# Kernel optimization log

Measured on AMD Instinct MI355X. Metric: run time of the kernel, lower is better.

Reference implementation:

```python
import jax, jax.numpy as jnp
import numpy as np

N_EMBED = 1024
HEAD_SIZE = 128

def setup_inputs() -> dict:
    key = jax.random.key(0)
    k1, k2, k3, k4 = jax.random.split(key, 4)
    x = jax.random.normal(k1, (8, 2048, N_EMBED), dtype=jnp.float32)
    # torch.nn.Linear default init: U(-1/sqrt(in), 1/sqrt(in)); stored as [out, in],
    # we store transposed [in, out] for x @ W.
    bound = 1.0 / np.sqrt(N_EMBED)
    Wk = jax.random.uniform(k2, (N_EMBED, HEAD_SIZE), jnp.float32, -bound, bound)
    Wq = jax.random.uniform(k3, (N_EMBED, HEAD_SIZE), jnp.float32, -bound, bound)
    Wv = jax.random.uniform(k4, (N_EMBED, HEAD_SIZE), jnp.float32, -bound, bound)
    return {"x": x, "Wk": Wk, "Wq": Wq, "Wv": Wv}

def reference(x, Wk, Wq, Wv):
    # x: [B, T, E]
    k = jnp.einsum('bte,eh->bth', x, Wk)  # [B, T, H]
    q = jnp.einsum('bte,eh->bth', x, Wq)
    v = jnp.einsum('bte,eh->bth', x, Wv)
    scale = 1.0 / np.sqrt(HEAD_SIZE).astype(np.float32)
    wei = jnp.einsum('bqh,bkh->bqk', q, k) * scale  # [B, T, T]
    wei = jax.nn.softmax(wei, axis=-1)
    out = jnp.einsum('bqk,bkh->bqh', wei, v)  # [B, T, H]
    return out
```

## Files before the change

kernel.cpp:

```cpp
#include <hip/hip_runtime.h>

#define BATCH 8
#define TLEN 2048
#define EMB 1024
#define HDIM 128
#define SCALE 0.08838834764831845f
#define NSPLIT 4

typedef _Float16 f16x8 __attribute__((ext_vector_type(8)));
typedef _Float16 f16x4 __attribute__((ext_vector_type(4)));
typedef float f32x4 __attribute__((ext_vector_type(4)));

static __device__ __forceinline__ f32x4 mfma16(f16x8 a, f16x8 b, f32x4 c) {
    return __builtin_amdgcn_mfma_f32_16x16x32_f16(a, b, c, 0, 0, 0);
}

__global__ void prep_w(const float* __restrict__ Wk, const float* __restrict__ Wq,
                       const float* __restrict__ Wv, _Float16* __restrict__ wtf) {
    int g = blockIdx.x * 256 + threadIdx.x;
    int lane = g & 63;
    int kstep = (g >> 6) & 31;
    int ntile = g >> 11;
    int n = ntile * 16 + (lane & 15);
    int sel = n >> 7;
    int h = n & 127;
    const float* W = (sel == 0) ? Wk : (sel == 1) ? Wq : Wv;
    int kbase = kstep * 32 + (lane >> 4) * 8;
    f16x8 o;
#pragma unroll
    for (int j = 0; j < 8; j++) {
        float v = W[(size_t)(kbase + j) * HDIM + h];
        if (sel == 1) v *= SCALE;
        o[j] = (_Float16)v;
    }
    *(f16x8*)&wtf[(size_t)g * 8] = o;
}

#define XPITCH 1048
__global__ __launch_bounds__(256) void prep_x(const float* __restrict__ x,
                                              _Float16* __restrict__ xf) {
    __shared__ _Float16 ls[16 * XPITCH];
    const int t = threadIdx.x;
    const int mtile = blockIdx.x;
    const float* src = x + (size_t)mtile * 16 * EMB;
#pragma unroll
    for (int i = 0; i < 16; i++) {
        int f = t + i * 256;
        int row = f >> 8;
        int col = (f & 255) * 4;
        float4 v = *(const float4*)&src[(size_t)row * EMB + col];
        f16x4 h;
        h[0] = (_Float16)v.x; h[1] = (_Float16)v.y;
        h[2] = (_Float16)v.z; h[3] = (_Float16)v.w;
        *(f16x4*)&ls[row * XPITCH + col] = h;
    }
    __syncthreads();
    _Float16* dst = xf + (size_t)mtile * 32 * 512;
#pragma unroll
    for (int i = 0; i < 8; i++) {
        int u = t + i * 256;
        int kstep = u >> 6;
        int lane = u & 63;
        int kcol = kstep * 32 + (lane >> 4) * 8;
        f16x8 v = *(const f16x8*)&ls[(lane & 15) * XPITCH + kcol];
        *(f16x8*)&dst[(size_t)u * 8] = v;
    }
}

__global__ __launch_bounds__(512, 2) void proj_kernel(
        const _Float16* __restrict__ xf, const _Float16* __restrict__ wtf,
        _Float16* __restrict__ kb, _Float16* __restrict__ qb, _Float16* __restrict__ vbT) {
    const int t = threadIdx.x;
    const int wv = t >> 6;
    const int lane = t & 63;
    const int m16 = lane & 15;
    const int quad = lane >> 4;
    const int mhalf = (wv >> 2) * 32;
    const int nq = wv & 3;
    const int n0 = nq * 96;
    const int m0 = blockIdx.x * 64;

    const f32x4 zero4 = {0.f, 0.f, 0.f, 0.f};
    f32x4 acc[2][6];
#pragma unroll
    for (int mt = 0; mt < 2; mt++)
#pragma unroll
        for (int nt = 0; nt < 6; nt++) acc[mt][nt] = zero4;

    const _Float16* xq = &xf[(size_t)(blockIdx.x * 4 + (wv >> 2) * 2) * 32 * 512
                             + (size_t)lane * 8];
    const _Float16* wq = &wtf[(size_t)(nq * 6) * 32 * 512 + (size_t)lane * 8];

#pragma unroll 8
    for (int kstep = 0; kstep < 32; kstep++) {
        f16x8 af[2];
#pragma unroll
        for (int mt = 0; mt < 2; mt++)
            af[mt] = *(const f16x8*)&xq[(size_t)(mt * 32 + kstep) * 512];
        f16x8 bf[6];
#pragma unroll
        for (int nt = 0; nt < 6; nt++)
            bf[nt] = *(const f16x8*)&wq[(size_t)(nt * 32 + kstep) * 512];
#pragma unroll
        for (int nt = 0; nt < 6; nt++) {
            acc[0][nt] = mfma16(af[0], bf[nt], acc[0][nt]);
            acc[1][nt] = mfma16(af[1], bf[nt], acc[1][nt]);
        }
    }
#pragma unroll
    for (int nt = 0; nt < 6; nt++) {
        int n = n0 + nt * 16 + m16;
        int nsel = n >> 7;
        int h = n & 127;
        if (nsel < 2) {
            _Float16* dst = (nsel == 0) ? kb : qb;
#pragma unroll
            for (int mt = 0; mt < 2; mt++)
#pragma unroll
                for (int r = 0; r < 4; r++) {
                    int mg = m0 + mhalf + mt * 16 + quad * 4 + r;
                    dst[(size_t)mg * HDIM + h] = (_Float16)acc[mt][nt][r];
                }
        } else {
#pragma unroll
            for (int mt = 0; mt < 2; mt++) {
                int mg = m0 + mhalf + mt * 16 + quad * 4;
                int bb = mg >> 11, tok = mg & 2047;
                f16x4 pk;
#pragma unroll
                for (int r = 0; r < 4; r++) pk[r] = (_Float16)acc[mt][nt][r];
                *(f16x4*)&vbT[((size_t)bb * HDIM + h) * TLEN + tok] = pk;
            }
        }
    }
}

__global__ __launch_bounds__(256, 3) void attn_kernel(
        const _Float16* __restrict__ qb, const _Float16* __restrict__ kb,
        const _Float16* __restrict__ vbT,
        _Float16* __restrict__ po, float* __restrict__ pl) {
    __shared__ _Float16 kls[64 * 132];
    __shared__ _Float16 vtl[128 * 68];
    __shared__ _Float16 pls[4 * 32 * 72];
    const int t = threadIdx.x;
    const int qt = blockIdx.x;
    const int b = blockIdx.y;
    const int sp = blockIdx.z;
    const int wv = t >> 6;
    const int lane = t & 63;
    const int m16 = lane & 15;
    const int quad = lane >> 4;
    const int q0 = qt * 128 + wv * 32;
    _Float16* pw = pls + wv * (32 * 72);

    f16x8 qf[2][4];
#pragma unroll
    for (int mt = 0; mt < 2; mt++)
#pragma unroll
        for (int ks = 0; ks < 4; ks++)
            qf[mt][ks] = *(const f16x8*)
                &qb[((size_t)b * TLEN + q0 + mt * 16 + m16) * HDIM + ks * 32 + quad * 8];

    const f32x4 zero4 = {0.f, 0.f, 0.f, 0.f};
    f32x4 o[2][8];
    float lacc[2] = {0.f, 0.f};
#pragma unroll
    for (int mt = 0; mt < 2; mt++)
#pragma unroll
        for (int nt = 0; nt < 8; nt++) o[mt][nt] = zero4;

    for (int kt = sp * 8; kt < sp * 8 + 8; kt++) {
        const int k0 = kt * 64;
        f16x8 kreg[4];
#pragma unroll
        for (int rep = 0; rep < 4; rep++) {
            int u = t + rep * 256;
            kreg[rep] = *(const f16x8*)
                &kb[((size_t)b * TLEN + k0 + (u >> 4)) * HDIM + (u & 15) * 8];
        }
        __syncthreads();
#pragma unroll
        for (int rep = 0; rep < 4; rep++) {
            int u = t + rep * 256;
            *(f16x8*)&kls[(u >> 4) * 132 + (u & 15) * 8] = kreg[rep];
        }
#pragma unroll
        for (int rep = 0; rep < 4; rep++) {
            int u = t + rep * 256;
            f16x8 v = *(const f16x8*)
                &vbT[((size_t)b * HDIM + (u >> 3)) * TLEN + k0 + (u & 7) * 8];
            *(f16x8*)&vtl[(u >> 3) * 68 + (u & 7) * 8] = v;
        }
        __syncthreads();
#pragma unroll
        for (int kt_ = 0; kt_ < 4; kt_++) {
            f32x4 st0 = zero4, st1 = zero4;
#pragma unroll
            for (int ks = 0; ks < 4; ks++) {
                f16x8 kf = *(const f16x8*)&kls[(kt_ * 16 + m16) * 132 + ks * 32 + quad * 8];
                st0 = mfma16(kf, qf[0][ks], st0);
                st1 = mfma16(kf, qf[1][ks], st1);
            }
            f16x4 p0, p1;
#pragma unroll
            for (int r = 0; r < 4; r++) {
                float e0 = __expf(st0[r]);
                float e1 = __expf(st1[r]);
                lacc[0] += e0;
                lacc[1] += e1;
                p0[r] = (_Float16)e0;
                p1[r] = (_Float16)e1;
            }
            *(f16x4*)&pw[m16 * 72 + kt_ * 16 + quad * 4] = p0;
            *(f16x4*)&pw[(16 + m16) * 72 + kt_ * 16 + quad * 4] = p1;
        }
        f16x8 ap[2][2];
#pragma unroll
        for (int mt = 0; mt < 2; mt++)
#pragma unroll
            for (int kc = 0; kc < 2; kc++)
                ap[mt][kc] = *(const f16x8*)&pw[(mt * 16 + m16) * 72 + kc * 32 + quad * 8];
#pragma unroll
        for (int nt = 0; nt < 8; nt++) {
            f16x8 b0 = *(const f16x8*)&vtl[(nt * 16 + m16) * 68 + quad * 8];
            f16x8 b1 = *(const f16x8*)&vtl[(nt * 16 + m16) * 68 + 32 + quad * 8];
            o[0][nt] = mfma16(ap[0][0], b0, o[0][nt]);
            o[0][nt] = mfma16(ap[0][1], b1, o[0][nt]);
            o[1][nt] = mfma16(ap[1][0], b0, o[1][nt]);
            o[1][nt] = mfma16(ap[1][1], b1, o[1][nt]);
        }
    }
#pragma unroll
    for (int mt = 0; mt < 2; mt++) {
        lacc[mt] += __shfl_xor(lacc[mt], 16);
        lacc[mt] += __shfl_xor(lacc[mt], 32);
    }
#pragma unroll
    for (int mt = 0; mt < 2; mt++) {
        if (quad == 0)
            pl[((size_t)(sp * BATCH + b)) * TLEN + q0 + mt * 16 + m16] = lacc[mt];
#pragma unroll
        for (int r = 0; r < 4; r++) {
            int row = q0 + mt * 16 + quad * 4 + r;
            size_t prow = ((size_t)(sp * BATCH + b)) * TLEN + row;
#pragma unroll
            for (int nt = 0; nt < 8; nt++)
                po[prow * HDIM + nt * 16 + m16] = (_Float16)o[mt][nt][r];
        }
    }
}

__global__ void combine_kernel(const _Float16* __restrict__ po, const float* __restrict__ pl,
                               float* __restrict__ out) {
    int g = blockIdx.x * 256 + threadIdx.x;
    int row = g >> 5;
    int part = g & 31;
    int bb = row >> 11;
    int tok = row & 2047;
    float L = 0.f;
    float4 acc = {0.f, 0.f, 0.f, 0.f};
#pragma unroll
    for (int s = 0; s < NSPLIT; s++) {
        size_t prow = ((size_t)(s * BATCH + bb)) * TLEN + tok;
        L += pl[prow];
        f16x4 p = *(const f16x4*)&po[prow * HDIM + part * 4];
        acc.x += (float)p[0]; acc.y += (float)p[1];
        acc.z += (float)p[2]; acc.w += (float)p[3];
    }
    float inv = 1.f / L;
    float4 res = {acc.x * inv, acc.y * inv, acc.z * inv, acc.w * inv};
    *(float4*)&out[(size_t)row * HDIM + part * 4] = res;
}

extern "C" void kernel_launch(void* const* d_in, const int* in_sizes, int n_in,
                              void* d_out, int out_size, void* d_ws, size_t ws_size,
                              hipStream_t stream) {
    const float* x  = (const float*)d_in[0];
    const float* Wk = (const float*)d_in[1];
    const float* Wq = (const float*)d_in[2];
    const float* Wv = (const float*)d_in[3];
    float* out = (float*)d_out;
    char* ws = (char*)d_ws;
    _Float16* wtf = (_Float16*)(ws);
    _Float16* xf  = (_Float16*)(ws + (1ull << 20));
    _Float16* kb  = (_Float16*)(ws + (33ull << 20));
    _Float16* qb  = (_Float16*)(ws + (37ull << 20));
    _Float16* vbT = (_Float16*)(ws + (41ull << 20));
    _Float16* po  = (_Float16*)(ws + (45ull << 20));
    float* pl = (float*)(ws + (61ull << 20));

    prep_w<<<dim3(192), dim3(256), 0, stream>>>(Wk, Wq, Wv, wtf);
    prep_x<<<dim3(1024), dim3(256), 0, stream>>>(x, xf);
    proj_kernel<<<dim3(256), dim3(512), 0, stream>>>(xf, wtf, kb, qb, vbT);
    attn_kernel<<<dim3(16, BATCH, NSPLIT), dim3(256), 0, stream>>>(qb, kb, vbT, po, pl);
    combine_kernel<<<dim3(2048), dim3(256), 0, stream>>>(po, pl, out);
}
```

Measured before the change: 163.9 us.

## Merge prep kernels, read K directly from global, repack split-K partial layout

Merges the weight and input conversion kernels into one launch to save a launch gap. The attention kernel drops the K tile from shared memory and reads K fragments straight from global memory, freeing LDS so occupancy can rise to 4 blocks per CU. Partial outputs are stored in an MFMA-fragment-native layout with contiguous 16-byte stores, and the combine kernel is rewritten to read that layout. The trade-off is that every wave now reloads K from global/L2 instead of sharing it, and the final output writes in combine become scattered scalar stores.

New measurement: 222.0 us. 35.4% more time.

```diff
diff --git a/kernel.cpp b/kernel.cpp
--- a/kernel.cpp
+++ b/kernel.cpp
@@ -15,55 +15,56 @@
     return __builtin_amdgcn_mfma_f32_16x16x32_f16(a, b, c, 0, 0, 0);
 }
 
-__global__ void prep_w(const float* __restrict__ Wk, const float* __restrict__ Wq,
-                       const float* __restrict__ Wv, _Float16* __restrict__ wtf) {
-    int g = blockIdx.x * 256 + threadIdx.x;
-    int lane = g & 63;
-    int kstep = (g >> 6) & 31;
-    int ntile = g >> 11;
-    int n = ntile * 16 + (lane & 15);
-    int sel = n >> 7;
-    int h = n & 127;
-    const float* W = (sel == 0) ? Wk : (sel == 1) ? Wq : Wv;
-    int kbase = kstep * 32 + (lane >> 4) * 8;
-    f16x8 o;
-#pragma unroll
-    for (int j = 0; j < 8; j++) {
-        float v = W[(size_t)(kbase + j) * HDIM + h];
-        if (sel == 1) v *= SCALE;
-        o[j] = (_Float16)v;
-    }
-    *(f16x8*)&wtf[(size_t)g * 8] = o;
-}
-
 #define XPITCH 1048
-__global__ __launch_bounds__(256) void prep_x(const float* __restrict__ x,
-                                              _Float16* __restrict__ xf) {
+__global__ __launch_bounds__(256) void prep_kernel(
+        const float* __restrict__ x, const float* __restrict__ Wk,
+        const float* __restrict__ Wq, const float* __restrict__ Wv,
+        _Float16* __restrict__ xf, _Float16* __restrict__ wtf) {
     __shared__ _Float16 ls[16 * XPITCH];
     const int t = threadIdx.x;
-    const int mtile = blockIdx.x;
-    const float* src = x + (size_t)mtile * 16 * EMB;
-#pragma unroll
-    for (int i = 0; i < 16; i++) {
-        int f = t + i * 256;
-        int row = f >> 8;
-        int col = (f & 255) * 4;
-        float4 v = *(const float4*)&src[(size_t)row * EMB + col];
-        f16x4 h;
-        h[0] = (_Float16)v.x; h[1] = (_Float16)v.y;
-        h[2] = (_Float16)v.z; h[3] = (_Float16)v.w;
-        *(f16x4*)&ls[row * XPITCH + col] = h;
-    }
-    __syncthreads();
-    _Float16* dst = xf + (size_t)mtile * 32 * 512;
-#pragma unroll
-    for (int i = 0; i < 8; i++) {
-        int u = t + i * 256;
-        int kstep = u >> 6;
-        int lane = u & 63;
-        int kcol = kstep * 32 + (lane >> 4) * 8;
-        f16x8 v = *(const f16x8*)&ls[(lane & 15) * XPITCH + kcol];
-        *(f16x8*)&dst[(size_t)u * 8] = v;
+    if (blockIdx.x < 1024) {
+        const int mtile = blockIdx.x;
+        const float* src = x + (size_t)mtile * 16 * EMB;
+#pragma unroll
+        for (int i = 0; i < 16; i++) {
+            int f = t + i * 256;
+            int row = f >> 8;
+            int col = (f & 255) * 4;
+            float4 v = *(const float4*)&src[(size_t)row * EMB + col];
+            f16x4 h;
+            h[0] = (_Float16)v.x; h[1] = (_Float16)v.y;
+            h[2] = (_Float16)v.z; h[3] = (_Float16)v.w;
+            *(f16x4*)&ls[row * XPITCH + col] = h;
+        }
+        __syncthreads();
+        _Float16* dst = xf + (size_t)mtile * 32 * 512;
+#pragma unroll
+        for (int i = 0; i < 8; i++) {
+            int u = t + i * 256;
+            int kstep = u >> 6;
+            int lane = u & 63;
+            int kcol = kstep * 32 + (lane >> 4) * 8;
+            f16x8 v = *(const f16x8*)&ls[(lane & 15) * XPITCH + kcol];
+            *(f16x8*)&dst[(size_t)u * 8] = v;
+        }
+    } else {
+        int g = (blockIdx.x - 1024) * 256 + t;
+        int lane = g & 63;
+        int kstep = (g >> 6) & 31;
+        int ntile = g >> 11;
+        int n = ntile * 16 + (lane & 15);
+        int sel = n >> 7;
+        int h = n & 127;
+        const float* W = (sel == 0) ? Wk : (sel == 1) ? Wq : Wv;
+        int kbase = kstep * 32 + (lane >> 4) * 8;
+        f16x8 o;
+#pragma unroll
+        for (int j = 0; j < 8; j++) {
+            float v = W[(size_t)(kbase + j) * HDIM + h];
+            if (sel == 1) v *= SCALE;
+            o[j] = (_Float16)v;
+        }
+        *(f16x8*)&wtf[(size_t)g * 8] = o;
     }
 }
 
@@ -135,11 +136,10 @@
     }
 }
 
-__global__ __launch_bounds__(256, 3) void attn_kernel(
+__global__ __launch_bounds__(256, 4) void attn_kernel(
         const _Float16* __restrict__ qb, const _Float16* __restrict__ kb,
         const _Float16* __restrict__ vbT,
         _Float16* __restrict__ po, float* __restrict__ pl) {
-    __shared__ _Float16 kls[64 * 132];
     __shared__ _Float16 vtl[128 * 68];
     __shared__ _Float16 pls[4 * 32 * 72];
     const int t = threadIdx.x;
@@ -169,27 +169,22 @@
 #pragma unroll
         for (int nt = 0; nt < 8; nt++) o[mt][nt] = zero4;
 
+    const _Float16* kbase = &kb[(size_t)b * TLEN * HDIM];
+
     for (int kt = sp * 8; kt < sp * 8 + 8; kt++) {
         const int k0 = kt * 64;
-        f16x8 kreg[4];
+        f16x8 vreg[4];
 #pragma unroll
         for (int rep = 0; rep < 4; rep++) {
             int u = t + rep * 256;
-            kreg[rep] = *(const f16x8*)
-                &kb[((size_t)b * TLEN + k0 + (u >> 4)) * HDIM + (u & 15) * 8];
+            vreg[rep] = *(const f16x8*)
+                &vbT[((size_t)b * HDIM + (u >> 3)) * TLEN + k0 + (u & 7) * 8];
         }
         __syncthreads();
 #pragma unroll
         for (int rep = 0; rep < 4; rep++) {
             int u = t + rep * 256;
-            *(f16x8*)&kls[(u >> 4) * 132 + (u & 15) * 8] = kreg[rep];
-        }
-#pragma unroll
-        for (int rep = 0; rep < 4; rep++) {
-            int u = t + rep * 256;
-            f16x8 v = *(const f16x8*)
-                &vbT[((size_t)b * HDIM + (u >> 3)) * TLEN + k0 + (u & 7) * 8];
-            *(f16x8*)&vtl[(u >> 3) * 68 + (u & 7) * 8] = v;
+            *(f16x8*)&vtl[(u >> 3) * 68 + (u & 7) * 8] = vreg[rep];
         }
         __syncthreads();
 #pragma unroll
@@ -197,7 +192,8 @@
             f32x4 st0 = zero4, st1 = zero4;
 #pragma unroll
             for (int ks = 0; ks < 4; ks++) {
-                f16x8 kf = *(const f16x8*)&kls[(kt_ * 16 + m16) * 132 + ks * 32 + quad * 8];
+                f16x8 kf = *(const f16x8*)
+                    &kbase[(size_t)(k0 + kt_ * 16 + m16) * HDIM + ks * 32 + quad * 8];
                 st0 = mfma16(kf, qf[0][ks], st0);
                 st1 = mfma16(kf, qf[1][ks], st1);
             }
@@ -234,42 +230,64 @@
     for (int mt = 0; mt < 2; mt++) {
         lacc[mt] += __shfl_xor(lacc[mt], 16);
         lacc[mt] += __shfl_xor(lacc[mt], 32);
-    }
-#pragma unroll
-    for (int mt = 0; mt < 2; mt++) {
         if (quad == 0)
             pl[((size_t)(sp * BATCH + b)) * TLEN + q0 + mt * 16 + m16] = lacc[mt];
+    }
+    const int cid = (b * 16 + qt) * 4 + wv;
+    _Float16* pbase = &po[((size_t)(sp * 512 + cid) * 8) * 512 + (size_t)lane * 8];
+#pragma unroll
+    for (int j = 0; j < 8; j++) {
+        f16x8 v;
+#pragma unroll
+        for (int i = 0; i < 8; i++)
+            v[i] = (_Float16)o[j >> 2][(j & 3) * 2 + (i >> 2)][i & 3];
+        *(f16x8*)&pbase[(size_t)j * 512] = v;
+    }
+}
+
+__global__ __launch_bounds__(256) void combine_kernel(
+        const _Float16* __restrict__ po, const float* __restrict__ pl,
+        float* __restrict__ out) {
+    int g = blockIdx.x * 256 + threadIdx.x;
+    int cid = g >> 6;
+    int lane = g & 63;
+    int b = cid >> 6;
+    int qt = (cid >> 2) & 15;
+    int wv = cid & 3;
+    int m16 = lane & 15;
+    int quad = lane >> 4;
+    int q0 = qt * 128 + wv * 32;
+    float Linv[2][4];
+#pragma unroll
+    for (int mt = 0; mt < 2; mt++)
 #pragma unroll
         for (int r = 0; r < 4; r++) {
             int row = q0 + mt * 16 + quad * 4 + r;
-            size_t prow = ((size_t)(sp * BATCH + b)) * TLEN + row;
-#pragma unroll
-            for (int nt = 0; nt < 8; nt++)
-                po[prow * HDIM + nt * 16 + m16] = (_Float16)o[mt][nt][r];
-        }
-    }
-}
-
-__global__ void combine_kernel(const _Float16* __restrict__ po, const float* __restrict__ pl,
-                               float* __restrict__ out) {
-    int g = blockIdx.x * 256 + threadIdx.x;
-    int row = g >> 5;
-    int part = g & 31;
-    int bb = row >> 11;
-    int tok = row & 2047;
-    float L = 0.f;
-    float4 acc = {0.f, 0.f, 0.f, 0.f};
-#pragma unroll
-    for (int s = 0; s < NSPLIT; s++) {
-        size_t prow = ((size_t)(s * BATCH + bb)) * TLEN + tok;
-        L += pl[prow];
-        f16x4 p = *(const f16x4*)&po[prow * HDIM + part * 4];
-        acc.x += (float)p[0]; acc.y += (float)p[1];
-        acc.z += (float)p[2]; acc.w += (float)p[3];
-    }
-    float inv = 1.f / L;
-    float4 res = {acc.x * inv, acc.y * inv, acc.z * inv, acc.w * inv};
-    *(float4*)&out[(size_t)row * HDIM + part * 4] = res;
+            float L = 0.f;
+#pragma unroll
+            for (int s = 0; s < NSPLIT; s++)
+                L += pl[((size_t)(s * BATCH + b)) * TLEN + row];
+            Linv[mt][r] = 1.f / L;
+        }
+#pragma unroll
+    for (int j = 0; j < 8; j++) {
+        float acc[8] = {0.f, 0.f, 0.f, 0.f, 0.f, 0.f, 0.f, 0.f};
+#pragma unroll
+        for (int s = 0; s < NSPLIT; s++) {
+            f16x8 p = *(const f16x8*)
+                &po[((size_t)(s * 512 + cid) * 8 + j) * 512 + (size_t)lane * 8];
+#pragma unroll
+            for (int i = 0; i < 8; i++) acc[i] += (float)p[i];
+        }
+        int mt = j >> 2;
+#pragma unroll
+        for (int i = 0; i < 8; i++) {
+            int nt = (j & 3) * 2 + (i >> 2);
+            int r = i & 3;
+            int row = q0 + mt * 16 + quad * 4 + r;
+            out[((size_t)b * TLEN + row) * HDIM + nt * 16 + m16] = acc[i] * Linv[mt][r];
+        }
+    }
 }
 
 extern "C" void kernel_launch(void* const* d_in, const int* in_sizes, int n_in,
@@ -289,9 +307,8 @@
     _Float16* po  = (_Float16*)(ws + (45ull << 20));
     float* pl = (float*)(ws + (61ull << 20));
 
-    prep_w<<<dim3(192), dim3(256), 0, stream>>>(Wk, Wq, Wv, wtf);
-    prep_x<<<dim3(1024), dim3(256), 0, stream>>>(x, xf);
+    prep_kernel<<<dim3(1216), dim3(256), 0, stream>>>(x, Wk, Wq, Wv, xf, wtf);
     proj_kernel<<<dim3(256), dim3(512), 0, stream>>>(xf, wtf, kb, qb, vbT);
     attn_kernel<<<dim3(16, BATCH, NSPLIT), dim3(256), 0, stream>>>(qb, kb, vbT, po, pl);
-    combine_kernel<<<dim3(2048), dim3(256), 0, stream>>>(po, pl, out);
-}
+    combine_kernel<<<dim3(128), dim3(256), 0, stream>>>(po, pl, out);
+}
```
